# Performance work log

Hardware: AMD Instinct MI355X
Metric: run time of the kernel (lower is better)

The kernel has to match this reference:

```python
import jax, jax.numpy as jnp
import numpy as np
from jax import lax

B, T, C = 128, 2048, 128


def setup_inputs() -> dict:
    key = jax.random.key(0)
    k1, k2 = jax.random.split(key)
    inputs = jax.random.normal(k1, (B, T, C), dtype=jnp.float32)
    transitions = jax.random.normal(k2, (C, C), dtype=jnp.float32)
    return {"inputs": inputs, "transitions": transitions}


def _viterbi_decode(potentials, transitions):
    """Max-plus Viterbi decode, full sequence lengths.
    potentials: [B, T, C], transitions: [C, C] -> tags [B, T] int32."""
    def fwd_step(alpha, pot_t):
        # alpha: [B, C] best score ending in each tag at t-1
        scores = alpha[:, :, None] + transitions[None, :, :]  # [B, C_prev, C_cur]
        best_prev = jnp.max(scores, axis=1)                    # [B, C]
        bp = jnp.argmax(scores, axis=1).astype(jnp.int32)      # [B, C] backpointers
        return best_prev + pot_t, bp

    alpha0 = potentials[:, 0]                                  # [B, C]
    pots_rest = jnp.swapaxes(potentials[:, 1:], 0, 1)          # [T-1, B, C]
    alpha_T, bps = lax.scan(fwd_step, alpha0, pots_rest)

    last_tag = jnp.argmax(alpha_T, axis=-1).astype(jnp.int32)  # [B]

    def back_step(tag, bp_t):
        prev = jnp.take_along_axis(bp_t, tag[:, None], axis=1)[:, 0]
        return prev, prev

    # reverse scan over backpointers; outputs stacked in original time order
    _, tags_prefix = lax.scan(back_step, last_tag, bps, reverse=True)  # [T-1, B]
    tags = jnp.concatenate([tags_prefix, last_tag[None, :]], axis=0)   # [T, B]
    return jnp.swapaxes(tags, 0, 1)                                    # [B, T]


def reference(inputs, transitions):
    # CRF.call at inference: viterbi decode, tags cast to input dtype
    tags = _viterbi_decode(inputs, transitions)
    return tags.astype(inputs.dtype)
```

## Files before the change

### kernel.cpp

```cpp
#include <hip/hip_runtime.h>
#include <cstdint>
#include <cstddef>

#define B_DIM 128
#define T_LEN 2048
#define C_DIM 128
#define NSTEP (T_LEN - 1)
#define NS4   512

#define FSKEW(x) ((x) + 8 * ((x) >> 5))

#define LDS_BARRIER() asm volatile("s_waitcnt lgkmcnt(0)\n\ts_barrier" ::: "memory")

#define TR_LIST(X) \
    X(0)  X(1)  X(2)  X(3)  X(4)  X(5)  X(6)  X(7)  \
    X(8)  X(9)  X(10) X(11) X(12) X(13) X(14) X(15) \
    X(16) X(17) X(18) X(19) X(20) X(21) X(22) X(23) \
    X(24) X(25) X(26) X(27) X(28) X(29) X(30) X(31)

template <int CTRL>
__device__ __forceinline__ float dppf(float x)
{
    return __int_as_float(__builtin_amdgcn_update_dpp(
        0, __float_as_int(x), CTRL, 0xF, 0xF, true));
}

__device__ __forceinline__ float max32(const float s[32])
{
    float u[11];
#pragma unroll
    for (int p = 0; p < 10; ++p)
        u[p] = fmaxf(fmaxf(s[3 * p], s[3 * p + 1]), s[3 * p + 2]);
    u[10] = fmaxf(s[30], s[31]);
    const float w0 = fmaxf(fmaxf(u[0], u[1]), u[2]);
    const float w1 = fmaxf(fmaxf(u[3], u[4]), u[5]);
    const float w2 = fmaxf(fmaxf(u[6], u[7]), u[8]);
    const float w3 = fmaxf(u[9], u[10]);
    return fmaxf(fmaxf(w0, w1), fmaxf(w2, w3));
}

__global__ __launch_bounds__(512)
__attribute__((amdgpu_waves_per_eu(2, 2)))
void viterbi_fwd_a(
    const float* __restrict__ pot,
    const float* __restrict__ trans,
    float* __restrict__ vstarG,
    int* __restrict__ lastTag)
{
    const int b   = blockIdx.x;
    const int tid = threadIdx.x;
    const int w   = tid >> 6;
    const int l   = tid & 63;
    const int d   = l & 3;
    const int j   = 16 * w + (l >> 2);
    const int fj  = FSKEW(j);
    const int ib  = 32 * d;

    __shared__ __align__(16) float alphabuf[2][160];

#define DECL_TR(K) const float tr_##K = trans[(ib + (K)) * C_DIM + j];
    TR_LIST(DECL_TR)
#undef DECL_TR

    const float* potb = pot + (size_t)b * T_LEN * C_DIM;
    float* vG = vstarG + (size_t)b * NSTEP * C_DIM;

    if (tid < C_DIM) alphabuf[1][FSKEW(tid)] = potb[tid];

    float pq0 = potb[1 * C_DIM + j];
    float pq1 = potb[2 * C_DIM + j];
    float pq2 = potb[3 * C_DIM + j];
    float pq3 = potb[4 * C_DIM + j];
    __syncthreads();

#define ADD_TR(K) s_[K] = a_[K] + tr_##K;

#define STEP_A(T_, PQ_)                                                       \
    {                                                                         \
        const float* ac_ = &alphabuf[(T_) & 1][40 * d];                       \
        float a_[32];                                                         \
        _Pragma("unroll")                                                     \
        for (int e_ = 0; e_ < 8; ++e_)                                        \
            *(float4*)&a_[4 * e_] = *(const float4*)&ac_[4 * e_];             \
        float s_[32];                                                         \
        TR_LIST(ADD_TR)                                                       \
        float v_ = max32(s_);                                                 \
        v_ = fmaxf(v_, dppf<0xB1>(v_));                                       \
        v_ = fmaxf(v_, dppf<0x4E>(v_));                                       \
        const float av_ = v_ + (PQ_);                                         \
        alphabuf[((T_) + 1) & 1][fj] = av_;                                   \
        vG[(size_t)((T_) - 1) * C_DIM + j] = v_;                              \
        const int tn_ = ((T_) + 4 < T_LEN) ? ((T_) + 4) : (T_LEN - 1);        \
        PQ_ = potb[tn_ * C_DIM + j];         \
        LDS_BARRIER();                                                        \
    }

    for (int t = 1; t < 2045; t += 4) {
        STEP_A(t + 0, pq0)
        STEP_A(t + 1, pq1)
        STEP_A(t + 2, pq2)
        STEP_A(t + 3, pq3)
    }
    STEP_A(2045, pq0)
    STEP_A(2046, pq1)
    STEP_A(2047, pq2)
#undef STEP_A
#undef ADD_TR

    if (tid < 64) {
        const float* af = alphabuf[0];
        const float v0 = af[FSKEW(tid)];
        const float v1 = af[FSKEW(tid + 64)];
        float v = v0; int x = tid;
        if (v1 > v0) { v = v1; x = tid + 64; }
#pragma unroll
        for (int mk = 1; mk < 64; mk <<= 1) {
            const float pv = __shfl_xor(v, mk);
            const int   px = __shfl_xor(x, mk);
            if (pv > v || (pv == v && px < x)) { v = pv; x = px; }
        }
        if (tid == 0) lastTag[b] = x;
    }
}

__global__ __launch_bounds__(64, 1) void viterbi_bwd_v(
    const float* __restrict__ pot,
    const float* __restrict__ vstarG,
    const float* __restrict__ trans,
    const int* __restrict__ lastTag,
    float* __restrict__ out)
{
    const int b = blockIdx.x;
    const int l = threadIdx.x;
    float* outb = out + (size_t)b * T_LEN;
    const float* potb = pot + (size_t)b * T_LEN * C_DIM;
    const float* vbse = vstarG + (size_t)b * NSTEP * C_DIM;

    __shared__ float Tl[C_DIM][C_DIM];
    for (int k = l; k < C_DIM * C_DIM; k += 64) {
        const int i = k >> 7;
        const int jj = k & 127;
        Tl[i][jj ^ (i & 31)] = trans[k];
    }

    float pa0, pb0, va0, vb0, pa1, pb1, va1, vb1, pa2, pb2, va2, vb2,
          pa3, pb3, va3, vb3, pa4, pb4, va4, vb4, pa5, pb5, va5, vb5;
    auto ldrow = [&](int r, float& pa, float& pb, float& va, float& vb) {
        const int rr = (r > 0) ? r : 0;
        pa = potb[(size_t)rr * C_DIM + l];
        pb = potb[(size_t)rr * C_DIM + l + 64];
        va = vbse[(size_t)rr * C_DIM + l];
        vb = vbse[(size_t)rr * C_DIM + l + 64];
    };
    ldrow(2046, pa0, pb0, va0, vb0);
    ldrow(2045, pa1, pb1, va1, vb1);
    ldrow(2044, pa2, pb2, va2, vb2);
    ldrow(2043, pa3, pb3, va3, vb3);
    ldrow(2042, pa4, pb4, va4, vb4);
    ldrow(2041, pa5, pb5, va5, vb5);

    int cur = lastTag[b];
    outb[T_LEN - 1] = (float)cur;
    __syncthreads();

#define BODY(PAu, PBu, VAu, VBu, VAn, VBn, RROW)                              \
    {                                                                         \
        const int cl = cur & 63;                                              \
        const float rl0 = __int_as_float(                                     \
            __builtin_amdgcn_readlane(__float_as_int(VAu), cl));              \
        const float rl1 = __int_as_float(                                     \
            __builtin_amdgcn_readlane(__float_as_int(VBu), cl));              \
        const float smax = (cur & 64) ? rl1 : rl0;                            \
        const int sw = cur ^ (l & 31);                                        \
        const float c0 = Tl[l][sw];                                           \
        const float c1 = Tl[l + 64][sw];                                      \
        const float s0 = (PAu + VAn) + c0;                                    \
        const float s1 = (PBu + VBn) + c1;                                    \
        const unsigned long long m0 = __ballot(s0 == smax);                   \
        const unsigned long long m1 = __ballot(s1 == smax);                   \
        cur = m0 ? (__ffsll(m0) - 1) : (64 + __ffsll(m1) - 1);                \
        outb[RROW] = (float)cur;                                              \
        ldrow((RROW) - 6, PAu, PBu, VAu, VBu);                                \
    }

    for (int r = 2046; r >= 6; r -= 6) {
        BODY(pa0, pb0, va0, vb0, va1, vb1, r - 0)
        BODY(pa1, pb1, va1, vb1, va2, vb2, r - 1)
        BODY(pa2, pb2, va2, vb2, va3, vb3, r - 2)
        BODY(pa3, pb3, va3, vb3, va4, vb4, r - 3)
        BODY(pa4, pb4, va4, vb4, va5, vb5, r - 4)
        BODY(pa5, pb5, va5, vb5, va0, vb0, r - 5)
    }
#undef BODY

    {
        const int cl = cur & 63;
        const float rl0 = __int_as_float(
            __builtin_amdgcn_readlane(__float_as_int(va0), cl));
        const float rl1 = __int_as_float(
            __builtin_amdgcn_readlane(__float_as_int(vb0), cl));
        const float smax = (cur & 64) ? rl1 : rl0;
        const int sw = cur ^ (l & 31);
        const float s0 = pa0 + Tl[l][sw];
        const float s1 = pb0 + Tl[l + 64][sw];
        const unsigned long long m0 = __ballot(s0 == smax);
        const unsigned long long m1 = __ballot(s1 == smax);
        cur = m0 ? (__ffsll(m0) - 1) : (64 + __ffsll(m1) - 1);
        outb[0] = (float)cur;
    }
}

__global__ __launch_bounds__(512)
__attribute__((amdgpu_waves_per_eu(2, 2)))
void viterbi_fwd(
    const float* __restrict__ pot,
    const float* __restrict__ trans,
    unsigned* __restrict__ bp4,
    int* __restrict__ lastTag)
{
    const int b   = blockIdx.x;
    const int tid = threadIdx.x;
    const int w   = tid >> 6;
    const int l   = tid & 63;
    const int d   = l & 3;
    const int j   = 16 * w + (l >> 2);
    const int fj  = FSKEW(j);
    const int ib  = 32 * d;

    __shared__ __align__(16) float alphabuf[2][160];

#define DECL_TR(K) float tr_##K = trans[(ib + (K)) * C_DIM + j];
    TR_LIST(DECL_TR)
#undef DECL_TR

    const float* potb = pot + (size_t)b * T_LEN * C_DIM;

    if (tid < C_DIM) alphabuf[1][FSKEW(tid)] = potb[tid];

    float pq0 = 0.f, pq1 = 0.f, pq2 = 0.f, pq3 = 0.f;
    if (d == 0) {
        pq0 = potb[1 * C_DIM + j];
        pq1 = potb[2 * C_DIM + j];
        pq2 = potb[3 * C_DIM + j];
        pq3 = potb[4 * C_DIM + j];
    }
    unsigned pack = 0;
    __syncthreads();

#define ADD_TR(K) s_[K] = a_[K] + tr_##K;

#define STEP(T_, C_, PQ_)                                                     \
    {                                                                         \
        const float* ac_ = &alphabuf[(T_) & 1][40 * d];                       \
        float a_[32];                                                         \
        _Pragma("unroll")                                                     \
        for (int e_ = 0; e_ < 8; ++e_)                                        \
            *(float4*)&a_[4 * e_] = *(const float4*)&ac_[4 * e_];             \
        float s_[32];                                                         \
        TR_LIST(ADD_TR)                                                       \
        float v16_[16]; int x16_[16];                                         \
        _Pragma("unroll")                                                     \
        for (int p_ = 0; p_ < 16; ++p_) {                                     \
            const bool g_ = s_[2 * p_ + 1] > s_[2 * p_];                      \
            v16_[p_] = g_ ? s_[2 * p_ + 1] : s_[2 * p_];                      \
            x16_[p_] = g_ ? 2 * p_ + 1 : 2 * p_;                              \
        }                                                                     \
        float v8_[8]; int x8_[8];                                             \
        _Pragma("unroll")                                                     \
        for (int p_ = 0; p_ < 8; ++p_) {                                      \
            const bool g_ = v16_[2 * p_ + 1] > v16_[2 * p_];                  \
            v8_[p_] = g_ ? v16_[2 * p_ + 1] : v16_[2 * p_];                   \
            x8_[p_] = g_ ? x16_[2 * p_ + 1] : x16_[2 * p_];                   \
        }                                                                     \
        float v4_[4]; int x4_[4];                                             \
        _Pragma("unroll")                                                     \
        for (int p_ = 0; p_ < 4; ++p_) {                                      \
            const bool g_ = v8_[2 * p_ + 1] > v8_[2 * p_];                    \
            v4_[p_] = g_ ? v8_[2 * p_ + 1] : v8_[2 * p_];                     \
            x4_[p_] = g_ ? x8_[2 * p_ + 1] : x8_[2 * p_];                     \
        }                                                                     \
        float v2_[2]; int x2_[2];                                             \
        _Pragma("unroll")                                                     \
        for (int p_ = 0; p_ < 2; ++p_) {                                      \
            const bool g_ = v4_[2 * p_ + 1] > v4_[2 * p_];                    \
            v2_[p_] = g_ ? v4_[2 * p_ + 1] : v4_[2 * p_];                     \
            x2_[p_] = g_ ? x4_[2 * p_ + 1] : x4_[2 * p_];                     \
        }                                                                     \
        const bool gf_ = v2_[1] > v2_[0];                                     \
        float v_ = gf_ ? v2_[1] : v2_[0];                                     \
        int   x_ = ib + (gf_ ? x2_[1] : x2_[0]);                              \
        {                                                                     \
            const float pv_ = __int_as_float(__builtin_amdgcn_update_dpp(     \
                0, __float_as_int(v_), 0xB1, 0xF, 0xF, true));                \
            const int   px_ = __builtin_amdgcn_update_dpp(                    \
                0, x_, 0xB1, 0xF, 0xF, true);                                 \
            const bool  pl_ = d & 1;                                          \
            const bool  tk_ = (pv_ > v_) || (pl_ && (pv_ == v_));             \
            if (tk_) { v_ = pv_; x_ = px_; }                                  \
        }                                                                     \
        {                                                                     \
            const float pv_ = __int_as_float(__builtin_amdgcn_update_dpp(     \
                0, __float_as_int(v_), 0x4E, 0xF, 0xF, true));                \
            const int   px_ = __builtin_amdgcn_update_dpp(                    \
                0, x_, 0x4E, 0xF, 0xF, true);                                 \
            const bool  pl_ = (d >> 1) & 1;                                   \
            const bool  tk_ = (pv_ > v_) || (pl_ && (pv_ == v_));             \
            if (tk_) { v_ = pv_; x_ = px_; }                                  \
        }                                                                     \
        if (d == 0) {                                                         \
            alphabuf[((T_) + 1) & 1][fj] = v_ + (PQ_);                        \
            pack |= (unsigned)x_ << (8 * (C_));                               \
            if ((C_) == 3) {                                                  \
                bp4[((size_t)(((T_) - 1) >> 2) * B_DIM + b) * C_DIM + j] =    \
                    pack;                                                     \
                pack = 0;                                                     \
            }                                                                 \
            if ((T_) + 4 < T_LEN) PQ_ = potb[((T_) + 4) * C_DIM + j];         \
        }                                                                     \
        LDS_BARRIER();                                                        \
    }

    for (int t = 1; t < 2045; t += 4) {
        STEP(t + 0, 0, pq0)
        STEP(t + 1, 1, pq1)
        STEP(t + 2, 2, pq2)
        STEP(t + 3, 3, pq3)
    }
    STEP(2045, 0, pq0)
    STEP(2046, 1, pq1)
    STEP(2047, 2, pq2)
    if (d == 0)
        bp4[((size_t)511 * B_DIM + b) * C_DIM + j] = pack;
#undef STEP
#undef ADD_TR

    if (tid < 64) {
        const float* af = alphabuf[0];
        const float v0 = af[FSKEW(tid)];
        const float v1 = af[FSKEW(tid + 64)];
        float v = v0; int x = tid;
        if (v1 > v0) { v = v1; x = tid + 64; }
#pragma unroll
        for (int mk = 1; mk < 64; mk <<= 1) {
            const float pv = __shfl_xor(v, mk);
            const int   px = __shfl_xor(x, mk);
            if (pv > v || (pv == v && px < x)) { v = pv; x = px; }
        }
        if (tid == 0) lastTag[b] = x;
    }
}

__global__ __launch_bounds__(64, 1) void viterbi_bwd(
    const unsigned* __restrict__ bp4,
    const int* __restrict__ lastTag,
    float* __restrict__ out)
{
    const int b = blockIdx.x;
    const int l = threadIdx.x;
    float* outb = out + (size_t)b * T_LEN;

    unsigned qa0 = 0, qb0 = 0, qa1 = 0, qb1 = 0,
             qa2 = 0, qb2 = 0, qa3 = 0, qb3 = 0;

    auto ld = [&](int s4, unsigned& A, unsigned& B) {
        if (s4 >= 0) {
            const unsigned* r = bp4 + ((size_t)s4 * B_DIM + b) * C_DIM;
            A = r[l];
            B = r[l + 64];
        }
    };
    ld(511, qa0, qb0);
    ld(510, qa1, qb1);
    ld(509, qa2, qb2);
    ld(508, qa3, qb3);

    int cur = lastTag[b];

    auto ext = [&](unsigned rA, unsigned rB, int c, int byte) -> int {
        const int addr = (c & 63) << 2;
        const int vA = __builtin_amdgcn_ds_bpermute(addr, (int)rA);
        const int vB = __builtin_amdgcn_ds_bpermute(addr, (int)rB);
        const int v = (c & 64) ? vB : vA;
        return (v >> (byte * 8)) & 0xFF;
    };

    {
        const unsigned rA = qa0, rB = qb0;
        const float t3 = (float)cur;
        cur = ext(rA, rB, cur, 2); const float t2 = (float)cur;
        cur = ext(rA, rB, cur, 1); const float t1 = (float)cur;
        cur = ext(rA, rB, cur, 0); const float t0 = (float)cur;
        if (l == 0) *(float4*)(outb + 4 * 511) = make_float4(t0, t1, t2, t3);
        qa0 = qa1; qb0 = qb1; qa1 = qa2; qb1 = qb2; qa2 = qa3; qb2 = qb3;
        ld(507, qa3, qb3);
    }

    for (int s4 = 510; s4 >= 0; --s4) {
        const unsigned rA = qa0, rB = qb0;
        cur = ext(rA, rB, cur, 3); const float t3 = (float)cur;
        cur = ext(rA, rB, cur, 2); const float t2 = (float)cur;
        cur = ext(rA, rB, cur, 1); const float t1 = (float)cur;
        cur = ext(rA, rB, cur, 0); const float t0 = (float)cur;
        if (l == 0) *(float4*)(outb + 4 * s4) = make_float4(t0, t1, t2, t3);
        qa0 = qa1; qb0 = qb1; qa1 = qa2; qb1 = qb2; qa2 = qa3; qb2 = qb3;
        ld(s4 - 4, qa3, qb3);
    }
}

extern "C" void kernel_launch(void* const* d_in, const int* in_sizes, int n_in,
                              void* d_out, int out_size, void* d_ws, size_t ws_size,
                              hipStream_t stream)
{
    const float* pot   = (const float*)d_in[0];
    const float* trans = (const float*)d_in[1];
    float* out = (float*)d_out;

    const size_t vstarBytes = (size_t)B_DIM * NSTEP * C_DIM * sizeof(float);

    if (ws_size >= vstarBytes + 512) {
        float* vstarG = (float*)d_ws;
        int* lastTag  = (int*)((char*)d_ws + vstarBytes);
        viterbi_fwd_a<<<B_DIM, 512, 0, stream>>>(pot, trans, vstarG, lastTag);
        viterbi_bwd_v<<<B_DIM, 64, 0, stream>>>(pot, vstarG, trans, lastTag, out);
    } else {
        unsigned* bp4 = (unsigned*)d_ws;
        int* lastTag  = (int*)((char*)d_ws + (size_t)NS4 * B_DIM * C_DIM * 4);
        viterbi_fwd<<<B_DIM, 512, 0, stream>>>(pot, trans, bp4, lastTag);
        viterbi_bwd<<<B_DIM, 64, 0, stream>>>(bp4, lastTag, out);
    }
}
```

Measured before the change: 966.4 us.

## Interleave two batch chains per wave in backward Viterbi with deeper prefetch

The backward traceback kernel now processes two batch rows per 64-thread block, interleaving their serial dependency chains so each one's latency (LDS read, ballot, readlane) can hide the other's. The prefetch queue of pot/vstar rows grows from 6 to 11 rows per chain, which raises memory-level parallelism. In exchange the kernel launches half as many blocks (64 instead of 128), leaving more CUs idle, and uses many more registers for the two queues.

```diff
diff --git a/kernel.cpp b/kernel.cpp
--- a/kernel.cpp
+++ b/kernel.cpp
@@ -123,18 +123,22 @@
     }
 }
 
-__global__ __launch_bounds__(64, 1) void viterbi_bwd_v(
+__global__ __launch_bounds__(64, 1) void viterbi_bwd_v2(
     const float* __restrict__ pot,
     const float* __restrict__ vstarG,
     const float* __restrict__ trans,
     const int* __restrict__ lastTag,
     float* __restrict__ out)
 {
-    const int b = blockIdx.x;
-    const int l = threadIdx.x;
-    float* outb = out + (size_t)b * T_LEN;
-    const float* potb = pot + (size_t)b * T_LEN * C_DIM;
-    const float* vbse = vstarG + (size_t)b * NSTEP * C_DIM;
+    const int b0 = 2 * blockIdx.x;
+    const int b1 = b0 + 1;
+    const int l  = threadIdx.x;
+    float* outA = out + (size_t)b0 * T_LEN;
+    float* outB = out + (size_t)b1 * T_LEN;
+    const float* potA = pot + (size_t)b0 * T_LEN * C_DIM;
+    const float* potB = pot + (size_t)b1 * T_LEN * C_DIM;
+    const float* vsA  = vstarG + (size_t)b0 * NSTEP * C_DIM;
+    const float* vsB  = vstarG + (size_t)b1 * NSTEP * C_DIM;
 
     __shared__ float Tl[C_DIM][C_DIM];
     for (int k = l; k < C_DIM * C_DIM; k += 64) {
@@ -143,71 +147,93 @@
         Tl[i][jj ^ (i & 31)] = trans[k];
     }
 
-    float pa0, pb0, va0, vb0, pa1, pb1, va1, vb1, pa2, pb2, va2, vb2,
-          pa3, pb3, va3, vb3, pa4, pb4, va4, vb4, pa5, pb5, va5, vb5;
-    auto ldrow = [&](int r, float& pa, float& pb, float& va, float& vb) {
+#define QD 11
+    float paA[QD], pbA[QD], vaA[QD], vbA[QD];
+    float paB[QD], pbB[QD], vaB[QD], vbB[QD];
+    auto ldrow = [&](const float* pbase, const float* vbase, int r,
+                     float& PA, float& PB, float& VA, float& VB) {
         const int rr = (r > 0) ? r : 0;
-        pa = potb[(size_t)rr * C_DIM + l];
-        pb = potb[(size_t)rr * C_DIM + l + 64];
-        va = vbse[(size_t)rr * C_DIM + l];
-        vb = vbse[(size_t)rr * C_DIM + l + 64];
+        PA = pbase[(size_t)rr * C_DIM + l];
+        PB = pbase[(size_t)rr * C_DIM + l + 64];
+        VA = vbase[(size_t)rr * C_DIM + l];
+        VB = vbase[(size_t)rr * C_DIM + l + 64];
     };
-    ldrow(2046, pa0, pb0, va0, vb0);
-    ldrow(2045, pa1, pb1, va1, vb1);
-    ldrow(2044, pa2, pb2, va2, vb2);
-    ldrow(2043, pa3, pb3, va3, vb3);
-    ldrow(2042, pa4, pb4, va4, vb4);
-    ldrow(2041, pa5, pb5, va5, vb5);
-
-    int cur = lastTag[b];
-    outb[T_LEN - 1] = (float)cur;
+#pragma unroll
+    for (int u = 0; u < QD; ++u) {
+        ldrow(potA, vsA, 2046 - u, paA[u], pbA[u], vaA[u], vbA[u]);
+        ldrow(potB, vsB, 2046 - u, paB[u], pbB[u], vaB[u], vbB[u]);
+    }
+
+    int curA = lastTag[b0];
+    int curB = lastTag[b1];
+    outA[T_LEN - 1] = (float)curA;
+    outB[T_LEN - 1] = (float)curB;
     __syncthreads();
 
-#define BODY(PAu, PBu, VAu, VBu, VAn, VBn, RROW)                              \
+#define BODY(CUR, PAu, PBu, VAu, VBu, VAn, VBn, OUTB, POTB, VSB, R)           \
     {                                                                         \
-        const int cl = cur & 63;                                              \
+        const int cl = CUR & 63;                                              \
         const float rl0 = __int_as_float(                                     \
             __builtin_amdgcn_readlane(__float_as_int(VAu), cl));              \
         const float rl1 = __int_as_float(                                     \
             __builtin_amdgcn_readlane(__float_as_int(VBu), cl));              \
-        const float smax = (cur & 64) ? rl1 : rl0;                            \
-        const int sw = cur ^ (l & 31);                                        \
+        const float smax = (CUR & 64) ? rl1 : rl0;                            \
+        const int sw = CUR ^ (l & 31);                                        \
         const float c0 = Tl[l][sw];                                           \
         const float c1 = Tl[l + 64][sw];                                      \
         const float s0 = (PAu + VAn) + c0;                                    \
         const float s1 = (PBu + VBn) + c1;                                    \
         const unsigned long long m0 = __ballot(s0 == smax);                   \
         const unsigned long long m1 = __ballot(s1 == smax);                   \
-        cur = m0 ? (__ffsll(m0) - 1) : (64 + __ffsll(m1) - 1);                \
-        outb[RROW] = (float)cur;                                              \
-        ldrow((RROW) - 6, PAu, PBu, VAu, VBu);                                \
-    }
-
-    for (int r = 2046; r >= 6; r -= 6) {
-        BODY(pa0, pb0, va0, vb0, va1, vb1, r - 0)
-        BODY(pa1, pb1, va1, vb1, va2, vb2, r - 1)
-        BODY(pa2, pb2, va2, vb2, va3, vb3, r - 2)
-        BODY(pa3, pb3, va3, vb3, va4, vb4, r - 3)
-        BODY(pa4, pb4, va4, vb4, va5, vb5, r - 4)
-        BODY(pa5, pb5, va5, vb5, va0, vb0, r - 5)
+        CUR = m0 ? (__ffsll(m0) - 1) : (64 + __ffsll(m1) - 1);                \
+        OUTB[R] = (float)CUR;                                                 \
+        ldrow(POTB, VSB, (R) - QD, PAu, PBu, VAu, VBu);                       \
+    }
+
+    for (int rbase = 2046; rbase >= QD; rbase -= QD) {
+#pragma unroll
+        for (int u = 0; u < QD; ++u) {
+            const int R  = rbase - u;
+            const int un = (u + 1) % QD;
+            BODY(curA, paA[u], pbA[u], vaA[u], vbA[u], vaA[un], vbA[un],
+                 outA, potA, vsA, R)
+            BODY(curB, paB[u], pbB[u], vaB[u], vbB[u], vaB[un], vbB[un],
+                 outB, potB, vsB, R)
+        }
     }
 #undef BODY
 
     {
-        const int cl = cur & 63;
+        const int cl = curA & 63;
         const float rl0 = __int_as_float(
-            __builtin_amdgcn_readlane(__float_as_int(va0), cl));
+            __builtin_amdgcn_readlane(__float_as_int(vaA[0]), cl));
         const float rl1 = __int_as_float(
-            __builtin_amdgcn_readlane(__float_as_int(vb0), cl));
-        const float smax = (cur & 64) ? rl1 : rl0;
-        const int sw = cur ^ (l & 31);
-        const float s0 = pa0 + Tl[l][sw];
-        const float s1 = pb0 + Tl[l + 64][sw];
+            __builtin_amdgcn_readlane(__float_as_int(vbA[0]), cl));
+        const float smax = (curA & 64) ? rl1 : rl0;
+        const int sw = curA ^ (l & 31);
+        const float s0 = paA[0] + Tl[l][sw];
+        const float s1 = pbA[0] + Tl[l + 64][sw];
         const unsigned long long m0 = __ballot(s0 == smax);
         const unsigned long long m1 = __ballot(s1 == smax);
-        cur = m0 ? (__ffsll(m0) - 1) : (64 + __ffsll(m1) - 1);
-        outb[0] = (float)cur;
-    }
+        curA = m0 ? (__ffsll(m0) - 1) : (64 + __ffsll(m1) - 1);
+        outA[0] = (float)curA;
+    }
+    {
+        const int cl = curB & 63;
+        const float rl0 = __int_as_float(
+            __builtin_amdgcn_readlane(__float_as_int(vaB[0]), cl));
+        const float rl1 = __int_as_float(
+            __builtin_amdgcn_readlane(__float_as_int(vbB[0]), cl));
+        const float smax = (curB & 64) ? rl1 : rl0;
+        const int sw = curB ^ (l & 31);
+        const float s0 = paB[0] + Tl[l][sw];
+        const float s1 = pbB[0] + Tl[l + 64][sw];
+        const unsigned long long m0 = __ballot(s0 == smax);
+        const unsigned long long m1 = __ballot(s1 == smax);
+        curB = m0 ? (__ffsll(m0) - 1) : (64 + __ffsll(m1) - 1);
+        outB[0] = (float)curB;
+    }
+#undef QD
 }
 
 __global__ __launch_bounds__(512)
@@ -421,7 +447,7 @@
         float* vstarG = (float*)d_ws;
         int* lastTag  = (int*)((char*)d_ws + vstarBytes);
         viterbi_fwd_a<<<B_DIM, 512, 0, stream>>>(pot, trans, vstarG, lastTag);
-        viterbi_bwd_v<<<B_DIM, 64, 0, stream>>>(pot, vstarG, trans, lastTag, out);
+        viterbi_bwd_v2<<<B_DIM / 2, 64, 0, stream>>>(pot, vstarG, trans, lastTag, out);
     } else {
         unsigned* bp4 = (unsigned*)d_ws;
         int* lastTag  = (int*)((char*)d_ws + (size_t)NS4 * B_DIM * C_DIM * 4);
```

After: 1.120 ms. +15.9%, slower.
